# Kernel optimization log

Hardware: AMD Instinct MI355X
Metric: run time of the kernel (lower is better)

Reference implementation:

```python
import jax, jax.numpy as jnp
import numpy as np

B, S, D, H = 4, 2048, 256, 8
HD = D // H
SCALE = float(np.sqrt(HD))  # temperature = head_dim ** 0.5


def setup_inputs() -> dict:
    key = jax.random.key(0)
    ks = jax.random.split(key, 12)
    w = lambda k, shape: jax.random.normal(k, shape, dtype=jnp.float32) * 0.05
    x = jax.random.normal(ks[0], (B, S, D), dtype=jnp.float32)
    adj = jax.random.randint(ks[1], (B, S, S), 0, 2, dtype=jnp.int32)
    return {
        "x": x,
        "adj": adj,
        "w_qkv": w(ks[2], (3 * D, D)),
        "b_qkv": jnp.zeros((3 * D,), jnp.float32),
        "ln_g": jnp.ones((D,), jnp.float32),
        "ln_b": jnp.zeros((D,), jnp.float32),
        "w_fc": w(ks[3], (D, D)),
        "b_fc": jnp.zeros((D,), jnp.float32),
        "w_z": w(ks[4], (D, D)),
        "b_z": jnp.full((D,), -2.0, jnp.float32),  # init_bias fills w_z bias with -2
        "u_z": w(ks[5], (D, D)),
        "w_r": w(ks[6], (D, D)),
        "u_r": w(ks[7], (D, D)),
        "w_g": w(ks[8], (D, D)),
        "u_g": w(ks[9], (D, D)),
    }


def reference(x, adj, w_qkv, b_qkv, ln_g, ln_b, w_fc, b_fc,
              w_z, b_z, u_z, w_r, u_r, w_g, u_g):
    residual = x
    # LayerNorm (eps=1e-5, torch default)
    mu = jnp.mean(x, axis=-1, keepdims=True)
    var = jnp.var(x, axis=-1, keepdims=True)
    xn = (x - mu) / jnp.sqrt(var + 1e-5) * ln_g + ln_b
    # fused QKV projection -> (B*H, S, 3*HD), batch-major over (b, h)
    qkv = xn @ w_qkv.T + b_qkv                       # [B,S,3D]
    qkv = qkv.reshape(B, S, H, 3 * HD).transpose(0, 2, 1, 3).reshape(B * H, S, 3 * HD)
    q, k, v = jnp.split(qkv, 3, axis=-1)
    # masked scaled dot-product attention (full NxN scores, as in original)
    attn = jnp.einsum('nqd,nkd->nqk', q, k) / SCALE  # [B*H,S,S]
    adj_r = jnp.repeat(adj, H, axis=0)               # batch-major, matches attn layout
    attn = jnp.where(adj_r == 0, -jnp.inf, attn)
    attn = jax.nn.softmax(attn, axis=-1)
    out = jnp.einsum('nqk,nkd->nqd', attn, v)        # [B*H,S,HD]
    # Faithful replication of torch's view(n_head, batch, ...) applied to
    # batch-major data (an ordering quirk in the original module).
    out = out.reshape(H, B, S, HD).transpose(1, 2, 0, 3).reshape(B, S, D)
    y = jax.nn.relu(out @ w_fc.T + b_fc)
    # GRU gate: x=residual, y=attention branch
    z = jax.nn.sigmoid(y @ w_z.T + b_z + residual @ u_z.T)
    r = jax.nn.sigmoid(y @ w_r.T + residual @ u_r.T)
    h_hat = jnp.tanh(y @ w_g.T + (r * residual) @ u_g.T)
    return (1.0 - z) * residual + z * h_hat
```

## Files before the change

### kernel.cpp

```cpp
#include <hip/hip_runtime.h>
#include <hip/hip_bf16.h>
#include <math.h>

#define B_  4
#define S_  2048
#define D_  256
#define H_  8
#define HD_ 32
#define QSCALE 0.25504175929589786f

typedef short  bf16x8 __attribute__((ext_vector_type(8)));
typedef float  f32x4  __attribute__((ext_vector_type(4)));
typedef float  f32x16 __attribute__((ext_vector_type(16)));
typedef unsigned short ushort_t;
typedef unsigned int   uint_t;

__device__ __forceinline__ ushort_t f2b(float f) {
    union { float f; unsigned u; } v; v.f = f;
    unsigned r = (v.u + 0x7FFFu + ((v.u >> 16) & 1u)) >> 16;
    return (ushort_t)r;
}
__device__ __forceinline__ float b2f(ushort_t s) {
    return __uint_as_float((uint_t)s << 16);
}
__device__ __forceinline__ f32x16 zero16() {
    f32x16 z;
#pragma unroll
    for (int i = 0; i < 16; ++i) z[i] = 0.f;
    return z;
}

__device__ __forceinline__ float wave_sum(float v) {
#pragma unroll
    for (int o = 32; o > 0; o >>= 1) v += __shfl_down(v, o, 64);
    return v;
}
__device__ __forceinline__ float block_sum256(float v, float* scr) {
    v = wave_sum(v);
    int lane = threadIdx.x & 63, wid = threadIdx.x >> 6;
    if (lane == 0) scr[wid] = v;
    __syncthreads();
    float r = scr[0] + scr[1] + scr[2] + scr[3];
    __syncthreads();
    return r;
}

#define WQ_SZ 196608
#define WS_SZ 65536
#define NB_ADJ 8192
#define NB_WC  2560
#define NB_LN  8192
__global__ __launch_bounds__(256)
void prep_kernel(const int* __restrict__ adj, uint_t* __restrict__ bits,
                 const float* __restrict__ w0, const float* __restrict__ w1,
                 const float* __restrict__ w2, const float* __restrict__ w3,
                 const float* __restrict__ w4, const float* __restrict__ w5,
                 const float* __restrict__ w6, const float* __restrict__ w7,
                 ushort_t* __restrict__ wout,
                 const float* __restrict__ x, const float* __restrict__ g,
                 const float* __restrict__ bb, ushort_t* __restrict__ xn_b) {
    __shared__ float scr[4];
    int blk = blockIdx.x, tid = threadIdx.x;
    if (blk < NB_ADJ) {
        int lane = tid & 63;
#pragma unroll
        for (int gp = 0; gp < 8; ++gp) {
            size_t i = ((size_t)blk * 8 + gp) * 256 + tid;
            unsigned long long m = __ballot(adj[i] != 0);
            size_t wbase = (((size_t)blk * 8 + gp) * 256 + (tid & ~63)) >> 5;
            if (lane == 0)  bits[wbase]     = (uint_t)m;
            if (lane == 32) bits[wbase + 1] = (uint_t)(m >> 32);
        }
    } else if (blk < NB_ADJ + NB_WC) {
        int idx = (blk - NB_ADJ) * 256 + tid;
        const float* src; int o;
        if (idx < WQ_SZ) { src = w0; o = idx; }
        else {
            int j = idx - WQ_SZ, seg = j >> 16; o = j & (WS_SZ - 1);
            src = (seg == 0) ? w1 : (seg == 1) ? w2 : (seg == 2) ? w3 :
                  (seg == 3) ? w4 : (seg == 4) ? w5 : (seg == 5) ? w6 : w7;
        }
        int j  = o & 7;
        int l  = (o >> 3) & 15;
        int qd = (o >> 7) & 3;
        int ks = (o >> 9) & 7;
        int ct = o >> 12;
        wout[idx] = f2b(src[(ct * 16 + l) * 256 + ks * 32 + qd * 8 + j]);
    } else {
        size_t base = (size_t)(blk - NB_ADJ - NB_WC) * D_;
        float v  = x[base + tid];
        float mu = block_sum256(v, scr) * (1.0f / D_);
        float d  = v - mu;
        float var = block_sum256(d * d, scr) * (1.0f / D_);
        float rstd = rsqrtf(var + 1e-5f);
        xn_b[base + tid] = f2b(d * rstd * g[tid] + bb[tid]);
    }
}

__global__ __launch_bounds__(256)
void gemm_qkv(const ushort_t* __restrict__ A, const ushort_t* __restrict__ Wf,
              const float* __restrict__ bias, ushort_t* __restrict__ outb,
              ushort_t* __restrict__ vT) {
    __shared__ ushort_t Sa[64][264];
    int tid = threadIdx.x;
    int wave = tid >> 6, lane = tid & 63, l = lane & 15, quad = lane >> 4;
    int wm = wave >> 1, wn = wave & 1;
    int m0 = blockIdx.y * 64, n0 = blockIdx.x * 64;
    {
        int row = tid >> 2, c0 = (tid & 3) * 64;
        const ushort_t* ap = A + (size_t)(m0 + row) * 256 + c0;
#pragma unroll
        for (int j = 0; j < 8; ++j)
            *(uint4*)&Sa[row][c0 + 8 * j] = ((const uint4*)ap)[j];
    }
    __syncthreads();

    bf16x8 af[2][8];
#pragma unroll
    for (int mt = 0; mt < 2; ++mt)
#pragma unroll
        for (int ks = 0; ks < 8; ++ks)
            af[mt][ks] = *(const bf16x8*)&Sa[wm * 32 + mt * 16 + l][ks * 32 + quad * 8];

    f32x4 acc[2][2];
#pragma unroll
    for (int i = 0; i < 2; ++i)
#pragma unroll
        for (int j = 0; j < 2; ++j) acc[i][j] = (f32x4){0.f, 0.f, 0.f, 0.f};

#pragma unroll
    for (int nt = 0; nt < 2; ++nt) {
        int ct = (n0 >> 4) + wn * 2 + nt;
        bf16x8 wfr[8];
#pragma unroll
        for (int ks = 0; ks < 8; ++ks)
            wfr[ks] = *(const bf16x8*)(Wf + (((size_t)ct * 8 + ks) * 64 + lane) * 8);
#pragma unroll
        for (int ks = 0; ks < 8; ++ks) {
            acc[0][nt] = __builtin_amdgcn_mfma_f32_16x16x32_bf16(af[0][ks], wfr[ks], acc[0][nt], 0, 0, 0);
            acc[1][nt] = __builtin_amdgcn_mfma_f32_16x16x32_bf16(af[1][ks], wfr[ks], acc[1][nt], 0, 0, 0);
        }
    }

    __syncthreads();
    ushort_t* So = &Sa[0][0];
#pragma unroll
    for (int nt = 0; nt < 2; ++nt) {
        int col = wn * 32 + nt * 16 + l;
        int gcol = n0 + col;
        float bv = bias[gcol];
        float qs = ((gcol % 96) < 32) ? QSCALE : 1.0f;
#pragma unroll
        for (int mt = 0; mt < 2; ++mt)
#pragma unroll
            for (int r = 0; r < 4; ++r) {
                int row = wm * 32 + mt * 16 + quad * 4 + r;
                So[row * 72 + col] = f2b((acc[mt][nt][r] + bv) * qs);
            }
    }
    __syncthreads();
    {
        int row = tid >> 2, seg = tid & 3;
        uint4 v0 = *(uint4*)&So[row * 72 + seg * 16];
        uint4 v1 = *(uint4*)&So[row * 72 + seg * 16 + 8];
        ushort_t* op = outb + (size_t)(m0 + row) * 768 + n0 + seg * 16;
        ((uint4*)op)[0] = v0;
        ((uint4*)op)[1] = v1;
    }

    int vs = n0 % 96;
    if (vs != 0) {
        int vloc = (vs == 64) ? 0 : 32;
        int h  = (n0 + vloc) / 96;
        int b  = m0 >> 11;
        int s0 = m0 & (S_ - 1);
        ushort_t* vstage = &Sa[0][0] + 8192;
        {
            int c = tid & 31, seg = tid >> 5;
            ushort_t tmp[8];
#pragma unroll
            for (int i = 0; i < 8; ++i)
                tmp[i] = So[(seg * 8 + i) * 72 + vloc + c];
            uint_t u[4];
#pragma unroll
            for (int i = 0; i < 4; ++i)
                u[i] = (uint_t)tmp[2 * i] | ((uint_t)tmp[2 * i + 1] << 16);
            *(uint4*)&vstage[c * 72 + seg * 8] = make_uint4(u[0], u[1], u[2], u[3]);
        }
        __syncthreads();
        {
            int d = tid >> 3, tseg = tid & 7;
            uint4 v = *(uint4*)&vstage[d * 72 + tseg * 8];
            *(uint4*)&vT[((size_t)(b * 8 + h) * 32 + d) * S_ + s0 + tseg * 8] = v;
        }
    }
}

__global__ __launch_bounds__(256)
void fused_gate(const ushort_t* __restrict__ attn_b, const float* __restrict__ xf,
                const ushort_t* __restrict__ wfc, const ushort_t* __restrict__ wz,
                const ushort_t* __restrict__ uz, const ushort_t* __restrict__ wr,
                const ushort_t* __restrict__ ur, const ushort_t* __restrict__ wg,
                const ushort_t* __restrict__ ug, const float* __restrict__ bfc,
                const float* __restrict__ bz, float* __restrict__ out) {
    __shared__ ushort_t Sa[16][264];
    __shared__ ushort_t Sx[16][264];
    __shared__ ushort_t Sy[16][264];
    __shared__ ushort_t St[16][264];
    int tid = threadIdx.x;
    int wave = tid >> 6, lane = tid & 63, l = lane & 15, quad = lane >> 4;
    int m0 = blockIdx.x * 16;
    int colbase = wave * 64;

    {
        int row = tid >> 4, c0 = (tid & 15) * 16;
        const ushort_t* ap = attn_b + (size_t)(m0 + row) * 256 + c0;
        uint4 a0 = ((const uint4*)ap)[0];
        uint4 a1 = ((const uint4*)ap)[1];
        *(uint4*)&Sa[row][c0] = a0;
        *(uint4*)&Sa[row][c0 + 8] = a1;
        const float4* xp = (const float4*)(xf + (size_t)(m0 + row) * 256 + c0);
        float4 f0 = xp[0], f1 = xp[1], f2_ = xp[2], f3 = xp[3];
        union { __hip_bfloat162 h[4]; uint4 u; } p0, p1;
        p0.h[0] = __float22bfloat162_rn(make_float2(f0.x, f0.y));
        p0.h[1] = __float22bfloat162_rn(make_float2(f0.z, f0.w));
        p0.h[2] = __float22bfloat162_rn(make_float2(f1.x, f1.y));
        p0.h[3] = __float22bfloat162_rn(make_float2(f1.z, f1.w));
        p1.h[0] = __float22bfloat162_rn(make_float2(f2_.x, f2_.y));
        p1.h[1] = __float22bfloat162_rn(make_float2(f2_.z, f2_.w));
        p1.h[2] = __float22bfloat162_rn(make_float2(f3.x, f3.y));
        p1.h[3] = __float22bfloat162_rn(make_float2(f3.z, f3.w));
        *(uint4*)&Sx[row][c0]     = p0.u;
        *(uint4*)&Sx[row][c0 + 8] = p1.u;
    }
    __syncthreads();

    {
        bf16x8 af[8];
#pragma unroll
        for (int ks = 0; ks < 8; ++ks)
            af[ks] = *(const bf16x8*)&Sa[l][ks * 32 + quad * 8];
        f32x4 ya[4];
#pragma unroll
        for (int nt = 0; nt < 4; ++nt) ya[nt] = (f32x4){0.f, 0.f, 0.f, 0.f};
#pragma unroll
        for (int nt = 0; nt < 4; ++nt) {
            size_t fb = ((size_t)(wave * 4 + nt) * 8) * 512 + lane * 8;
#pragma unroll
            for (int ks = 0; ks < 8; ++ks) {
                bf16x8 wfr = *(const bf16x8*)(wfc + fb + ks * 512);
                ya[nt] = __builtin_amdgcn_mfma_f32_16x16x32_bf16(af[ks], wfr, ya[nt], 0, 0, 0);
            }
        }
#pragma unroll
        for (int nt = 0; nt < 4; ++nt) {
            int col = colbase + nt * 16 + l;
            float bv = bfc[col];
#pragma unroll
            for (int r = 0; r < 4; ++r)
                Sy[quad * 4 + r][col] = f2b(fmaxf(ya[nt][r] + bv, 0.0f));
        }
    }
    __syncthreads();

    f32x4 az[4], ar[4], ag[4];
#pragma unroll
    for (int nt = 0; nt < 4; ++nt) {
        az[nt] = (f32x4){0.f, 0.f, 0.f, 0.f};
        ar[nt] = (f32x4){0.f, 0.f, 0.f, 0.f};
        ag[nt] = (f32x4){0.f, 0.f, 0.f, 0.f};
    }
#pragma unroll
    for (int nt = 0; nt < 4; ++nt) {
        size_t fb = ((size_t)(wave * 4 + nt) * 8) * 512 + lane * 8;
#pragma unroll
        for (int ks = 0; ks < 8; ++ks) {
            bf16x8 fy = *(const bf16x8*)&Sy[l][ks * 32 + quad * 8];
            bf16x8 fx = *(const bf16x8*)&Sx[l][ks * 32 + quad * 8];
            bf16x8 fz  = *(const bf16x8*)(wz + fb + ks * 512);
            bf16x8 fuz = *(const bf16x8*)(uz + fb + ks * 512);
            bf16x8 fr  = *(const bf16x8*)(wr + fb + ks * 512);
            bf16x8 fur = *(const bf16x8*)(ur + fb + ks * 512);
            bf16x8 fg  = *(const bf16x8*)(wg + fb + ks * 512);
            az[nt] = __builtin_amdgcn_mfma_f32_16x16x32_bf16(fy, fz,  az[nt], 0, 0, 0);
            az[nt] = __builtin_amdgcn_mfma_f32_16x16x32_bf16(fx, fuz, az[nt], 0, 0, 0);
            ar[nt] = __builtin_amdgcn_mfma_f32_16x16x32_bf16(fy, fr,  ar[nt], 0, 0, 0);
            ar[nt] = __builtin_amdgcn_mfma_f32_16x16x32_bf16(fx, fur, ar[nt], 0, 0, 0);
            ag[nt] = __builtin_amdgcn_mfma_f32_16x16x32_bf16(fy, fg,  ag[nt], 0, 0, 0);
        }
    }
#pragma unroll
    for (int nt = 0; nt < 4; ++nt) {
        int col = colbase + nt * 16 + l;
        float bzv = bz[col];
#pragma unroll
        for (int r = 0; r < 4; ++r) {
            int row = quad * 4 + r;
            az[nt][r] = 1.0f / (1.0f + __expf(-(az[nt][r] + bzv)));
            float rr  = 1.0f / (1.0f + __expf(-ar[nt][r]));
            St[row][col] = f2b(rr * b2f(Sx[row][col]));
        }
    }
    __syncthreads();

    f32x4 fcc[4];
#pragma unroll
    for (int nt = 0; nt < 4; ++nt) fcc[nt] = (f32x4){0.f, 0.f, 0.f, 0.f};
#pragma unroll
    for (int nt = 0; nt < 4; ++nt) {
        size_t fb = ((size_t)(wave * 4 + nt) * 8) * 512 + lane * 8;
#pragma unroll
        for (int ks = 0; ks < 8; ++ks) {
            bf16x8 ft = *(const bf16x8*)&St[l][ks * 32 + quad * 8];
            bf16x8 fu = *(const bf16x8*)(ug + fb + ks * 512);
            fcc[nt] = __builtin_amdgcn_mfma_f32_16x16x32_bf16(ft, fu, fcc[nt], 0, 0, 0);
        }
    }
#pragma unroll
    for (int nt = 0; nt < 4; ++nt) {
        int col = colbase + nt * 16 + l;
#pragma unroll
        for (int r = 0; r < 4; ++r) {
            int row = quad * 4 + r;
            float v = ag[nt][r] + fcc[nt][r];
            float e = __expf(2.0f * v);
            float h = 1.0f - 2.0f / (e + 1.0f);
            float zz = az[nt][r];
            size_t idx = (size_t)(m0 + row) * 256 + col;
            out[idx] = (1.0f - zz) * xf[idx] + zz * h;
        }
    }
}

__global__ __launch_bounds__(256)
void attn_kernel(const ushort_t* __restrict__ qkvb, const ushort_t* __restrict__ vT,
                 const uint_t* __restrict__ abits, ushort_t* __restrict__ attn_b) {
    __shared__ ushort_t Ks[2][64][40];
    __shared__ ushort_t Vt[2][32][72];

    int tid = threadIdx.x;
    int wave = tid >> 6, lane = tid & 63;
    int lane5 = lane & 31, hi = lane >> 5;
    int hsh8 = hi * 8;
    int pair = wave >> 1, half = wave & 1;

    int lid = blockIdx.y * 32 + blockIdx.x;
    int L   = (lid & 7) * 128 + (lid >> 3);
    int q0  = (L & 31) * 64;
    int n   = L >> 5;
    int b = n >> 3, h = n & 7;
    int bp = n & 3, hp = n >> 2;

    const ushort_t* base = qkvb + (size_t)b * S_ * 768 + h * 96;
    int qbase = pair * 32;
    int myq = q0 + qbase + lane5;
    const int kb = half * 32;

    bf16x8 qf1 = *(const bf16x8*)(base + (size_t)myq * 768 + hsh8);
    bf16x8 qf2 = *(const bf16x8*)(base + (size_t)myq * 768 + 16 + hsh8);

    bf16x8 ones;
#pragma unroll
    for (int i = 0; i < 8; ++i) ones[i] = (short)0x3F80;

    f32x16 oacc = zero16(), aones = zero16();

    int skey = tid >> 2, spart = tid & 3;
    int prow = (skey & ~12) | ((skey & 4) << 1) | ((skey & 8) >> 1);
    int kcol = (spart * 8) ^ (((prow >> 3) & 1) << 3);
    int vd = tid >> 3, vk = (tid & 7) * 8;
    const ushort_t* vptr = vT + ((size_t)n * 32 + vd) * S_ + vk;
    const uint_t* aptr = abits + ((size_t)b * S_ + myq) * 64 + half;

    uint_t aw = aptr[0];
    {
        uint4 k0v = *(const uint4*)(base + (size_t)skey * 768 + 32 + spart * 8);
        uint4 v0v = *(const uint4*)(vptr);
        *(uint4*)&Ks[0][prow][kcol] = k0v;
        *(uint4*)&Vt[0][vd][vk] = v0v;
    }
    uint4 kv = *(const uint4*)(base + (size_t)(64 + skey) * 768 + 32 + spart * 8);
    uint4 vv = *(const uint4*)(vptr + 64);
    __syncthreads();

    int b3 = (lane >> 3) & 1;

    for (int k0 = 0; k0 < S_; k0 += 64) {
        int cur = (k0 >> 6) & 1;
        bool more = (k0 + 64 < S_);
        uint_t awn;
        if (more) {
            *(uint4*)&Ks[cur ^ 1][prow][kcol] = kv;
            *(uint4*)&Vt[cur ^ 1][vd][vk] = vv;
            awn = aptr[(k0 + 64) >> 5];
            if (k0 + 128 < S_) {
                kv = *(const uint4*)(base + (size_t)(k0 + 128 + skey) * 768 + 32 + spart * 8);
                vv = *(const uint4*)(vptr + k0 + 128);
            }
        }

        bf16x8 kf1 = *(const bf16x8*)&Ks[cur][kb + lane5][(hi ^ b3) * 8];
        bf16x8 kf2 = *(const bf16x8*)&Ks[cur][kb + lane5][((2 + hi) ^ b3) * 8];
        f32x16 sc = zero16();
        sc = __builtin_amdgcn_mfma_f32_32x32x16_bf16(kf1, qf1, sc, 0, 0, 0);
        sc = __builtin_amdgcn_mfma_f32_32x32x16_bf16(kf2, qf2, sc, 0, 0, 0);

        uint_t wsub = aw >> hsh8;
        union { uint_t u[8]; bf16x8 v[2]; } pp;
#pragma unroll
        for (int i = 0; i < 8; ++i) {
            const int c = 2 * i + ((i >> 2) * 8);
            float e0 = exp2f(sc[2 * i]);
            float e1 = exp2f(sc[2 * i + 1]);
            uint_t m0 = (uint_t)((int)(wsub << (31 - c)) >> 31);
            uint_t m1 = (uint_t)((int)(wsub << (30 - c)) >> 31);
            e0 = __uint_as_float(__float_as_uint(e0) & m0);
            e1 = __uint_as_float(__float_as_uint(e1) & m1);
            union { __hip_bfloat162 b2; uint_t u; } p;
            p.b2 = __float22bfloat162_rn(make_float2(e0, e1));
            pp.u[i] = p.u;
        }

        bf16x8 vb1 = *(const bf16x8*)&Vt[cur][lane5][kb + hsh8];
        bf16x8 vb2 = *(const bf16x8*)&Vt[cur][lane5][kb + 16 + hsh8];

        __builtin_amdgcn_s_setprio(1);
        oacc  = __builtin_amdgcn_mfma_f32_32x32x16_bf16(pp.v[0], vb1,  oacc,  0, 0, 0);
        aones = __builtin_amdgcn_mfma_f32_32x32x16_bf16(pp.v[0], ones, aones, 0, 0, 0);
        oacc  = __builtin_amdgcn_mfma_f32_32x32x16_bf16(pp.v[1], vb2,  oacc,  0, 0, 0);
        aones = __builtin_amdgcn_mfma_f32_32x32x16_bf16(pp.v[1], ones, aones, 0, 0, 0);
        __builtin_amdgcn_s_setprio(0);

        if (more) aw = awn;
        __syncthreads();
    }

    float* red = (float*)&Ks[0][0][0];
    if (half) {
        float* dst = red + pair * 2048 + lane * 4;
#pragma unroll
        for (int j = 0; j < 4; ++j) {
            f32x4 t;
            t[0] = oacc[4 * j]; t[1] = oacc[4 * j + 1];
            t[2] = oacc[4 * j + 2]; t[3] = oacc[4 * j + 3];
            *(f32x4*)(dst + j * 256) = t;
        }
#pragma unroll
        for (int j = 0; j < 4; ++j) {
            f32x4 t;
            t[0] = aones[4 * j]; t[1] = aones[4 * j + 1];
            t[2] = aones[4 * j + 2]; t[3] = aones[4 * j + 3];
            *(f32x4*)(dst + (4 + j) * 256) = t;
        }
    }
    __syncthreads();
    if (!half) {
        const float* src = red + pair * 2048 + lane * 4;
#pragma unroll
        for (int j = 0; j < 4; ++j) {
            f32x4 t = *(const f32x4*)(src + j * 256);
            oacc[4 * j] += t[0]; oacc[4 * j + 1] += t[1];
            oacc[4 * j + 2] += t[2]; oacc[4 * j + 3] += t[3];
        }
#pragma unroll
        for (int j = 0; j < 4; ++j) {
            f32x4 t = *(const f32x4*)(src + (4 + j) * 256);
            aones[4 * j] += t[0]; aones[4 * j + 1] += t[1];
            aones[4 * j + 2] += t[2]; aones[4 * j + 3] += t[3];
        }
    }
    __syncthreads();

    ushort_t* Ost = &Ks[0][0][0];
    if (!half) {
#pragma unroll
        for (int r = 0; r < 16; ++r) {
            int qr = (r & 3) + 8 * (r >> 2) + 4 * hi;
            Ost[(qbase + qr) * 40 + lane5] = f2b(oacc[r] / aones[r]);
        }
    }
    __syncthreads();
    {
        int row = tid >> 2, part = tid & 3;
        uint4 v = *(uint4*)&Ost[row * 40 + part * 8];
        *(uint4*)&attn_b[((size_t)(bp * S_ + q0 + row)) * 256 + hp * 32 + part * 8] = v;
    }
}

extern "C" void kernel_launch(void* const* d_in, const int* in_sizes, int n_in,
                              void* d_out, int out_size, void* d_ws, size_t ws_size,
                              hipStream_t stream) {
    const float* x     = (const float*)d_in[0];
    const int*   adj   = (const int*)d_in[1];
    const float* w_qkv = (const float*)d_in[2];
    const float* b_qkv = (const float*)d_in[3];
    const float* ln_g  = (const float*)d_in[4];
    const float* ln_b  = (const float*)d_in[5];
    const float* w_fc  = (const float*)d_in[6];
    const float* b_fc  = (const float*)d_in[7];
    const float* w_z   = (const float*)d_in[8];
    const float* b_z   = (const float*)d_in[9];
    const float* u_z   = (const float*)d_in[10];
    const float* w_r   = (const float*)d_in[11];
    const float* u_r   = (const float*)d_in[12];
    const float* w_g   = (const float*)d_in[13];
    const float* u_g   = (const float*)d_in[14];
    float* out = (float*)d_out;

    const size_t TOK  = (size_t)B_ * S_;
    const size_t TOKD = TOK * D_;
    ushort_t* xn_b   = (ushort_t*)d_ws;
    ushort_t* qkv_b  = xn_b + TOKD;
    ushort_t* attn_b = qkv_b + TOK * 768;
    ushort_t* wb     = attn_b + TOKD;
    uint_t*   bits   = (uint_t*)(wb + WQ_SZ + 7 * WS_SZ);
    ushort_t* vTb    = (ushort_t*)(bits + (size_t)B_ * S_ * S_ / 32);

    ushort_t* wq_b  = wb;
    ushort_t* wfc_b = wb + WQ_SZ;
    ushort_t* wz_b  = wfc_b + WS_SZ;
    ushort_t* uz_b  = wz_b + WS_SZ;
    ushort_t* wr_b  = uz_b + WS_SZ;
    ushort_t* ur_b  = wr_b + WS_SZ;
    ushort_t* wg_b  = ur_b + WS_SZ;
    ushort_t* ug_b  = wg_b + WS_SZ;

    prep_kernel<<<NB_ADJ + NB_WC + NB_LN, 256, 0, stream>>>(
        adj, bits, w_qkv, w_fc, w_z, u_z, w_r, u_r, w_g, u_g, wb,
        x, ln_g, ln_b, xn_b);

    gemm_qkv<<<dim3(12, 128), 256, 0, stream>>>(xn_b, wq_b, b_qkv, qkv_b, vTb);

    attn_kernel<<<dim3(S_ / 64, B_ * H_), 256, 0, stream>>>(qkv_b, vTb, bits, attn_b);

    fused_gate<<<512, 256, 0, stream>>>(
        attn_b, x, wfc_b, wz_b, uz_b, wr_b, ur_b, wg_b, ug_b, b_fc, b_z, out);
}
```

Baseline: 236.5 us.

## Double attention key tile to 128, transpose adjacency bitmask layout, use native exp2

The attention loop now processes 128 keys per iteration instead of 64, with each wave handling two 32-key subtiles. This halves the number of __syncthreads barriers and global prefetch rounds per query block. The prep kernel writes the adjacency bitmask word-major (word index by 2048 queries), so per-lane mask loads in the attention kernel are coalesced across query lanes. exp2f is swapped for the hardware exp2 builtin. In exchange, LDS use per block grows to roughly double and registers per thread rise, which may lower occupancy.

```diff
diff --git a/kernel.cpp b/kernel.cpp
--- a/kernel.cpp
+++ b/kernel.cpp
@@ -63,13 +63,15 @@
     int blk = blockIdx.x, tid = threadIdx.x;
     if (blk < NB_ADJ) {
         int lane = tid & 63;
+        int b = blk >> 11, q = blk & 2047;
+        uint_t* outp = bits + ((size_t)b * 64) * 2048 + q;
 #pragma unroll
         for (int gp = 0; gp < 8; ++gp) {
             size_t i = ((size_t)blk * 8 + gp) * 256 + tid;
             unsigned long long m = __ballot(adj[i] != 0);
-            size_t wbase = (((size_t)blk * 8 + gp) * 256 + (tid & ~63)) >> 5;
-            if (lane == 0)  bits[wbase]     = (uint_t)m;
-            if (lane == 32) bits[wbase + 1] = (uint_t)(m >> 32);
+            int w = gp * 8 + ((tid & ~63) >> 5);
+            if (lane == 0)  outp[(size_t)w * 2048]       = (uint_t)m;
+            if (lane == 32) outp[(size_t)(w + 1) * 2048] = (uint_t)(m >> 32);
         }
     } else if (blk < NB_ADJ + NB_WC) {
         int idx = (blk - NB_ADJ) * 256 + tid;
@@ -335,8 +337,8 @@
 __global__ __launch_bounds__(256)
 void attn_kernel(const ushort_t* __restrict__ qkvb, const ushort_t* __restrict__ vT,
                  const uint_t* __restrict__ abits, ushort_t* __restrict__ attn_b) {
-    __shared__ ushort_t Ks[2][64][40];
-    __shared__ ushort_t Vt[2][32][72];
+    __shared__ ushort_t Ks[2][128][40];
+    __shared__ ushort_t Vt[2][32][136];
 
     int tid = threadIdx.x;
     int wave = tid >> 6, lane = tid & 63;
@@ -354,7 +356,7 @@
     const ushort_t* base = qkvb + (size_t)b * S_ * 768 + h * 96;
     int qbase = pair * 32;
     int myq = q0 + qbase + lane5;
-    const int kb = half * 32;
+    const int kofs = half * 64;
 
     bf16x8 qf1 = *(const bf16x8*)(base + (size_t)myq * 768 + hsh8);
     bf16x8 qf2 = *(const bf16x8*)(base + (size_t)myq * 768 + 16 + hsh8);
@@ -365,73 +367,91 @@
 
     f32x16 oacc = zero16(), aones = zero16();
 
-    int skey = tid >> 2, spart = tid & 3;
+    int skey = tid >> 1, sj = tid & 1;
     int prow = (skey & ~12) | ((skey & 4) << 1) | ((skey & 8) >> 1);
-    int kcol = (spart * 8) ^ (((prow >> 3) & 1) << 3);
+    int pxor = ((prow >> 3) & 1) << 3;
     int vd = tid >> 3, vk = (tid & 7) * 8;
     const ushort_t* vptr = vT + ((size_t)n * 32 + vd) * S_ + vk;
-    const uint_t* aptr = abits + ((size_t)b * S_ + myq) * 64 + half;
-
-    uint_t aw = aptr[0];
+    const ushort_t* kptr = base + (size_t)skey * 768 + 32 + sj * 16;
+    const uint_t* tb = abits + ((size_t)b * 64) * 2048 + myq;
+
+    uint_t aw0 = tb[(size_t)(half * 2 + 0) * 2048];
+    uint_t aw1 = tb[(size_t)(half * 2 + 1) * 2048];
     {
-        uint4 k0v = *(const uint4*)(base + (size_t)skey * 768 + 32 + spart * 8);
-        uint4 v0v = *(const uint4*)(vptr);
-        *(uint4*)&Ks[0][prow][kcol] = k0v;
-        *(uint4*)&Vt[0][vd][vk] = v0v;
-    }
-    uint4 kv = *(const uint4*)(base + (size_t)(64 + skey) * 768 + 32 + spart * 8);
-    uint4 vv = *(const uint4*)(vptr + 64);
+        uint4 ka = *(const uint4*)(kptr);
+        uint4 kb_ = *(const uint4*)(kptr + 8);
+        uint4 va = *(const uint4*)(vptr);
+        uint4 vb_ = *(const uint4*)(vptr + 64);
+        *(uint4*)&Ks[0][prow][(sj * 16 + 0) ^ pxor] = ka;
+        *(uint4*)&Ks[0][prow][(sj * 16 + 8) ^ pxor] = kb_;
+        *(uint4*)&Vt[0][vd][vk] = va;
+        *(uint4*)&Vt[0][vd][vk + 64] = vb_;
+    }
+    uint4 kv0 = *(const uint4*)(kptr + (size_t)128 * 768);
+    uint4 kv1 = *(const uint4*)(kptr + (size_t)128 * 768 + 8);
+    uint4 vv0 = *(const uint4*)(vptr + 128);
+    uint4 vv1 = *(const uint4*)(vptr + 192);
     __syncthreads();
 
     int b3 = (lane >> 3) & 1;
 
-    for (int k0 = 0; k0 < S_; k0 += 64) {
-        int cur = (k0 >> 6) & 1;
-        bool more = (k0 + 64 < S_);
-        uint_t awn;
+    for (int k0 = 0; k0 < S_; k0 += 128) {
+        int cur = (k0 >> 7) & 1;
+        bool more = (k0 + 128 < S_);
+        uint_t awn0, awn1;
         if (more) {
-            *(uint4*)&Ks[cur ^ 1][prow][kcol] = kv;
-            *(uint4*)&Vt[cur ^ 1][vd][vk] = vv;
-            awn = aptr[(k0 + 64) >> 5];
-            if (k0 + 128 < S_) {
-                kv = *(const uint4*)(base + (size_t)(k0 + 128 + skey) * 768 + 32 + spart * 8);
-                vv = *(const uint4*)(vptr + k0 + 128);
+            *(uint4*)&Ks[cur ^ 1][prow][(sj * 16 + 0) ^ pxor] = kv0;
+            *(uint4*)&Ks[cur ^ 1][prow][(sj * 16 + 8) ^ pxor] = kv1;
+            *(uint4*)&Vt[cur ^ 1][vd][vk] = vv0;
+            *(uint4*)&Vt[cur ^ 1][vd][vk + 64] = vv1;
+            int wn = ((k0 + 128) >> 5) + half * 2;
+            awn0 = tb[(size_t)(wn + 0) * 2048];
+            awn1 = tb[(size_t)(wn + 1) * 2048];
+            if (k0 + 256 < S_) {
+                kv0 = *(const uint4*)(kptr + (size_t)(k0 + 256) * 768);
+                kv1 = *(const uint4*)(kptr + (size_t)(k0 + 256) * 768 + 8);
+                vv0 = *(const uint4*)(vptr + k0 + 256);
+                vv1 = *(const uint4*)(vptr + k0 + 320);
             }
         }
 
-        bf16x8 kf1 = *(const bf16x8*)&Ks[cur][kb + lane5][(hi ^ b3) * 8];
-        bf16x8 kf2 = *(const bf16x8*)&Ks[cur][kb + lane5][((2 + hi) ^ b3) * 8];
-        f32x16 sc = zero16();
-        sc = __builtin_amdgcn_mfma_f32_32x32x16_bf16(kf1, qf1, sc, 0, 0, 0);
-        sc = __builtin_amdgcn_mfma_f32_32x32x16_bf16(kf2, qf2, sc, 0, 0, 0);
-
-        uint_t wsub = aw >> hsh8;
-        union { uint_t u[8]; bf16x8 v[2]; } pp;
-#pragma unroll
-        for (int i = 0; i < 8; ++i) {
-            const int c = 2 * i + ((i >> 2) * 8);
-            float e0 = exp2f(sc[2 * i]);
-            float e1 = exp2f(sc[2 * i + 1]);
-            uint_t m0 = (uint_t)((int)(wsub << (31 - c)) >> 31);
-            uint_t m1 = (uint_t)((int)(wsub << (30 - c)) >> 31);
-            e0 = __uint_as_float(__float_as_uint(e0) & m0);
-            e1 = __uint_as_float(__float_as_uint(e1) & m1);
-            union { __hip_bfloat162 b2; uint_t u; } p;
-            p.b2 = __float22bfloat162_rn(make_float2(e0, e1));
-            pp.u[i] = p.u;
-        }
-
-        bf16x8 vb1 = *(const bf16x8*)&Vt[cur][lane5][kb + hsh8];
-        bf16x8 vb2 = *(const bf16x8*)&Vt[cur][lane5][kb + 16 + hsh8];
-
-        __builtin_amdgcn_s_setprio(1);
-        oacc  = __builtin_amdgcn_mfma_f32_32x32x16_bf16(pp.v[0], vb1,  oacc,  0, 0, 0);
-        aones = __builtin_amdgcn_mfma_f32_32x32x16_bf16(pp.v[0], ones, aones, 0, 0, 0);
-        oacc  = __builtin_amdgcn_mfma_f32_32x32x16_bf16(pp.v[1], vb2,  oacc,  0, 0, 0);
-        aones = __builtin_amdgcn_mfma_f32_32x32x16_bf16(pp.v[1], ones, aones, 0, 0, 0);
-        __builtin_amdgcn_s_setprio(0);
-
-        if (more) aw = awn;
+#pragma unroll
+        for (int kb2 = 0; kb2 < 2; ++kb2) {
+            const int kb = kofs + kb2 * 32;
+            bf16x8 kf1 = *(const bf16x8*)&Ks[cur][kb + lane5][(hi ^ b3) * 8];
+            bf16x8 kf2 = *(const bf16x8*)&Ks[cur][kb + lane5][((2 + hi) ^ b3) * 8];
+            f32x16 sc = zero16();
+            sc = __builtin_amdgcn_mfma_f32_32x32x16_bf16(kf1, qf1, sc, 0, 0, 0);
+            sc = __builtin_amdgcn_mfma_f32_32x32x16_bf16(kf2, qf2, sc, 0, 0, 0);
+
+            uint_t wsub = (kb2 ? aw1 : aw0) >> hsh8;
+            union { uint_t u[8]; bf16x8 v[2]; } pp;
+#pragma unroll
+            for (int i = 0; i < 8; ++i) {
+                const int c = 2 * i + ((i >> 2) * 8);
+                float e0 = __builtin_amdgcn_exp2f(sc[2 * i]);
+                float e1 = __builtin_amdgcn_exp2f(sc[2 * i + 1]);
+                uint_t m0 = (uint_t)((int)(wsub << (31 - c)) >> 31);
+                uint_t m1 = (uint_t)((int)(wsub << (30 - c)) >> 31);
+                e0 = __uint_as_float(__float_as_uint(e0) & m0);
+                e1 = __uint_as_float(__float_as_uint(e1) & m1);
+                union { __hip_bfloat162 b2; uint_t u; } p;
+                p.b2 = __float22bfloat162_rn(make_float2(e0, e1));
+                pp.u[i] = p.u;
+            }
+
+            bf16x8 vb1 = *(const bf16x8*)&Vt[cur][lane5][kb + hsh8];
+            bf16x8 vb2 = *(const bf16x8*)&Vt[cur][lane5][kb + 16 + hsh8];
+
+            __builtin_amdgcn_s_setprio(1);
+            oacc  = __builtin_amdgcn_mfma_f32_32x32x16_bf16(pp.v[0], vb1,  oacc,  0, 0, 0);
+            aones = __builtin_amdgcn_mfma_f32_32x32x16_bf16(pp.v[0], ones, aones, 0, 0, 0);
+            oacc  = __builtin_amdgcn_mfma_f32_32x32x16_bf16(pp.v[1], vb2,  oacc,  0, 0, 0);
+            aones = __builtin_amdgcn_mfma_f32_32x32x16_bf16(pp.v[1], ones, aones, 0, 0, 0);
+            __builtin_amdgcn_s_setprio(0);
+        }
+
+        if (more) { aw0 = awn0; aw1 = awn1; }
         __syncthreads();
     }
 
```

After: 223.6 us. -5.5%, faster.
